# Kernel optimization log

Hardware: AMD Instinct MI355X
Metric: run time of the kernel (lower is better)

Reference implementation:

```python
import jax, jax.numpy as jnp
import numpy as np


def setup_inputs() -> dict:
    key = jax.random.key(0)
    k1, k2, k3, k4 = jax.random.split(key, 4)
    B, C, H, W = 16, 64, 128, 128
    x = jax.random.normal(k1, (B, C, H, W), dtype=jnp.float32)
    y = jax.random.normal(k2, (B, C, H, W), dtype=jnp.float32)
    # nn.Parameter(torch.zeros(1)) in the original; use small random values so
    # the attention branch contributes (zeros would make it a pure residual).
    temperature1 = jax.random.normal(k3, (1,), dtype=jnp.float32) * 0.1
    temperature2 = jax.random.normal(k4, (1,), dtype=jnp.float32) * 0.1
    return {"x": x, "y": y, "temperature1": temperature1,
            "temperature2": temperature2, "num_heads": 4}


def _l2norm_lastdim(v):
    # F.normalize(v, dim=-1): v / max(||v||_2, eps)
    n = jnp.sqrt(jnp.sum(v * v, axis=-1, keepdims=True))
    return v / jnp.maximum(n, 1e-12)


def reference(x, y, temperature1, temperature2, num_heads):
    B, C, H, W = x.shape
    c = C // num_heads
    HW = H * W
    # b (head c) h w -> b head c (h w)
    xr = x.reshape(B, num_heads, c, HW)
    yr = y.reshape(B, num_heads, c, HW)

    # key_x normalized over (h w); key_y (b head (hw) c) normalized over dim=-2,
    # which is the same (h w) axis of yr in 'bhck' layout.
    key_x = _l2norm_lastdim(xr)
    key_y = _l2norm_lastdim(yr)
    # energy[b,h,c,d] = sum_k key_x[b,h,c,k] * key_y[b,h,d,k]  -> (B, head, c, c)
    energy = jnp.einsum('bhck,bhdk->bhcd', key_x, key_y)

    attn1 = jax.nn.softmax(energy, axis=-1)                        # (B,h,c,c)
    attn2 = jax.nn.softmax(energy.transpose(0, 1, 3, 2), axis=-1)  # (B,h,c,c)

    # y_att (b head (hw) c) = value_y @ attn1, then 'b head (h w) c -> b (head c) h w'
    # out[b,h,d,k] = sum_c attn1[b,h,c,d] * yr[b,h,c,k]
    y_att = jnp.einsum('bhcd,bhck->bhdk', attn1, yr).reshape(B, C, H, W)
    x_att = jnp.einsum('bhcd,bhck->bhdk', attn2, xr).reshape(B, C, H, W)

    y_ = temperature1[0] * y_att + x
    x_ = temperature2[0] * x_att + y
    return jnp.concatenate((x_, y_), axis=1)  # (B, 2C, H, W)
```

## Files before the change

### kernel.cpp

```cpp
#include <hip/hip_runtime.h>

#define HW    16384
#define CPH   16
#define NBH   64
#define KSLICE 2048
#define TKT   256
#define LS    260
#define KPT   4

#define WS_SX   16384
#define WS_SY   17408
#define WS_W    18432
#define WS_ZERO_BYTES (18432 * 4)

__global__ __launch_bounds__(256) void gram_kernel(
    const float* __restrict__ x,
    const float* __restrict__ y,
    float* __restrict__ ws)
{
    __shared__ float xs[16 * LS];
    __shared__ float ys[16 * LS];
    __shared__ float Gs[256];
    __shared__ float sxs[16], sys[16];

    const int blk = blockIdx.x;
    const int bh  = blk >> 3;
    const int ks  = (blk & 7) * KSLICE;
    const int t   = threadIdx.x;

    Gs[t] = 0.f;
    if (t < 16) { sxs[t] = 0.f; sys[t] = 0.f; }

    const int c0 = t & 3;
    const int d0 = (t >> 2) & 3;
    const int g  = t >> 4;

    float acc[4][4];
    #pragma unroll
    for (int i = 0; i < 4; ++i)
        #pragma unroll
        for (int j = 0; j < 4; ++j) acc[i][j] = 0.f;
    float sqx[4] = {0.f, 0.f, 0.f, 0.f};
    float sqy[4] = {0.f, 0.f, 0.f, 0.f};

    const float* xb = x + (size_t)bh * CPH * HW + ks;
    const float* yb = y + (size_t)bh * CPH * HW + ks;

    for (int kt = 0; kt < KSLICE; kt += TKT) {
        __syncthreads();
        #pragma unroll
        for (int i = 0; i < 4; ++i) {
            int idx = i * 256 + t;
            int row = idx >> 6;
            int col = (idx & 63) * 4;
            float4 xv = *reinterpret_cast<const float4*>(xb + (size_t)row * HW + kt + col);
            float4 yv = *reinterpret_cast<const float4*>(yb + (size_t)row * HW + kt + col);
            *reinterpret_cast<float4*>(&xs[row * LS + col]) = xv;
            *reinterpret_cast<float4*>(&ys[row * LS + col]) = yv;
        }
        __syncthreads();

        #pragma unroll
        for (int kq = 0; kq < 16; kq += 4) {
            float4 xr[4], yr[4];
            #pragma unroll
            for (int i = 0; i < 4; ++i)
                xr[i] = *reinterpret_cast<const float4*>(&xs[(c0 + 4 * i) * LS + g * 16 + kq]);
            #pragma unroll
            for (int j = 0; j < 4; ++j)
                yr[j] = *reinterpret_cast<const float4*>(&ys[(d0 + 4 * j) * LS + g * 16 + kq]);
            #pragma unroll
            for (int i = 0; i < 4; ++i)
                #pragma unroll
                for (int j = 0; j < 4; ++j) {
                    acc[i][j] = fmaf(xr[i].x, yr[j].x, acc[i][j]);
                    acc[i][j] = fmaf(xr[i].y, yr[j].y, acc[i][j]);
                    acc[i][j] = fmaf(xr[i].z, yr[j].z, acc[i][j]);
                    acc[i][j] = fmaf(xr[i].w, yr[j].w, acc[i][j]);
                }
            if (d0 == 0) {
                #pragma unroll
                for (int i = 0; i < 4; ++i) {
                    sqx[i] = fmaf(xr[i].x, xr[i].x, sqx[i]);
                    sqx[i] = fmaf(xr[i].y, xr[i].y, sqx[i]);
                    sqx[i] = fmaf(xr[i].z, xr[i].z, sqx[i]);
                    sqx[i] = fmaf(xr[i].w, xr[i].w, sqx[i]);
                }
            }
            if (c0 == 0) {
                #pragma unroll
                for (int j = 0; j < 4; ++j) {
                    sqy[j] = fmaf(yr[j].x, yr[j].x, sqy[j]);
                    sqy[j] = fmaf(yr[j].y, yr[j].y, sqy[j]);
                    sqy[j] = fmaf(yr[j].z, yr[j].z, sqy[j]);
                    sqy[j] = fmaf(yr[j].w, yr[j].w, sqy[j]);
                }
            }
        }
    }

    #pragma unroll
    for (int i = 0; i < 4; ++i)
        #pragma unroll
        for (int j = 0; j < 4; ++j)
            atomicAdd(&Gs[(c0 + 4 * i) * 16 + (d0 + 4 * j)], acc[i][j]);
    if (d0 == 0) {
        #pragma unroll
        for (int i = 0; i < 4; ++i) atomicAdd(&sxs[c0 + 4 * i], sqx[i]);
    }
    if (c0 == 0) {
        #pragma unroll
        for (int j = 0; j < 4; ++j) atomicAdd(&sys[d0 + 4 * j], sqy[j]);
    }
    __syncthreads();
    atomicAdd(&ws[bh * 256 + t], Gs[t]);
    if (t < 16)       atomicAdd(&ws[WS_SX + bh * 16 + t], sxs[t]);
    else if (t < 32)  atomicAdd(&ws[WS_SY + bh * 16 + (t - 16)], sys[t - 16]);
}

__global__ __launch_bounds__(256) void softmax_kernel(
    float* __restrict__ ws,
    const float* __restrict__ t1p,
    const float* __restrict__ t2p)
{
    const int bh = blockIdx.x;
    const int t  = threadIdx.x;
    const int i  = t >> 4;
    const int j  = t & 15;

    __shared__ float Es[256];

    float nx = fmaxf(sqrtf(ws[WS_SX + bh * 16 + i]), 1e-12f);
    float ny = fmaxf(sqrtf(ws[WS_SY + bh * 16 + j]), 1e-12f);
    float e  = ws[bh * 256 + i * 16 + j] / (nx * ny);
    Es[t] = e;
    __syncthreads();

    float rm = -1e30f;
    #pragma unroll
    for (int r = 0; r < 16; ++r) rm = fmaxf(rm, Es[i * 16 + r]);
    float rs = 0.f;
    #pragma unroll
    for (int r = 0; r < 16; ++r) rs += expf(Es[i * 16 + r] - rm);
    float a1 = expf(e - rm) / rs;

    float cm = -1e30f;
    #pragma unroll
    for (int r = 0; r < 16; ++r) cm = fmaxf(cm, Es[r * 16 + j]);
    float cs = 0.f;
    #pragma unroll
    for (int r = 0; r < 16; ++r) cs += expf(Es[r * 16 + j] - cm);
    float v2 = expf(e - cm) / cs;

    const float t1 = t1p[0];
    const float t2 = t2p[0];

    float* W = ws + WS_W + bh * 512;
    W[(i * 16 + j) * 2 + 1] = t1 * a1;
    W[(j * 16 + i) * 2 + 0] = t2 * v2;
}

__global__ __launch_bounds__(256) void apply_kernel(
    const float* __restrict__ x,
    const float* __restrict__ y,
    const float* __restrict__ ws,
    float* __restrict__ out)
{
    const int CHUNKS = HW / (256 * KPT);
    const int blk   = blockIdx.x;
    const int bh    = blk / CHUNKS;
    const int chunk = blk % CHUNKS;
    const int t     = threadIdx.x;
    const int k0    = chunk * (256 * KPT) + t * KPT;

    __shared__ float2 Ws[256];
    Ws[t] = reinterpret_cast<const float2*>(ws + WS_W)[bh * 256 + t];
    __syncthreads();

    const int b = bh >> 2;
    const int h = bh & 3;

    const float* xbase = x + ((size_t)bh * CPH) * HW + k0;
    const float* ybase = y + ((size_t)bh * CPH) * HW + k0;

    float accx[16][KPT];
    float accy[16][KPT];
    #pragma unroll
    for (int d = 0; d < 16; ++d)
        #pragma unroll
        for (int j = 0; j < KPT; ++j) { accx[d][j] = 0.f; accy[d][j] = 0.f; }

    float4 xq = *reinterpret_cast<const float4*>(xbase);
    float4 yq = *reinterpret_cast<const float4*>(ybase);
    #pragma unroll
    for (int c = 0; c < 16; ++c) {
        float4 xn, yn;
        if (c < 15) {
            xn = *reinterpret_cast<const float4*>(xbase + (size_t)(c + 1) * HW);
            yn = *reinterpret_cast<const float4*>(ybase + (size_t)(c + 1) * HW);
        }
        float xv[KPT] = {xq.x, xq.y, xq.z, xq.w};
        float yv[KPT] = {yq.x, yq.y, yq.z, yq.w};
        #pragma unroll
        for (int d = 0; d < 16; ++d) {
            float2 w = Ws[c * 16 + d];
            #pragma unroll
            for (int j = 0; j < KPT; ++j) accx[d][j] = fmaf(w.x, xv[j], accx[d][j]);
            #pragma unroll
            for (int j = 0; j < KPT; ++j) accy[d][j] = fmaf(w.y, yv[j], accy[d][j]);
        }
        #pragma unroll
        for (int j = 0; j < KPT; ++j) accx[c][j] += yv[j];
        #pragma unroll
        for (int j = 0; j < KPT; ++j) accy[c][j] += xv[j];
        xq = xn; yq = yn;
    }

    const size_t obx = ((size_t)b * 128 + h * 16) * HW + k0;
    const size_t oby = obx + (size_t)64 * HW;
    #pragma unroll
    for (int d = 0; d < 16; ++d) {
        float4 px = make_float4(accx[d][0], accx[d][1], accx[d][2], accx[d][3]);
        float4 py = make_float4(accy[d][0], accy[d][1], accy[d][2], accy[d][3]);
        *reinterpret_cast<float4*>(out + obx + (size_t)d * HW) = px;
        *reinterpret_cast<float4*>(out + oby + (size_t)d * HW) = py;
    }
}

extern "C" void kernel_launch(void* const* d_in, const int* in_sizes, int n_in,
                              void* d_out, int out_size, void* d_ws, size_t ws_size,
                              hipStream_t stream) {
    const float* x  = (const float*)d_in[0];
    const float* y  = (const float*)d_in[1];
    const float* t1 = (const float*)d_in[2];
    const float* t2 = (const float*)d_in[3];
    float* ws  = (float*)d_ws;
    float* out = (float*)d_out;

    hipMemsetAsync(d_ws, 0, WS_ZERO_BYTES, stream);
    gram_kernel<<<NBH * 8, 256, 0, stream>>>(x, y, ws);
    softmax_kernel<<<NBH, 256, 0, stream>>>(ws, t1, t2);
    apply_kernel<<<NBH * (HW / (256 * KPT)), 256, 0, stream>>>(x, y, ws, out);
}
```

Baseline: 278.6 us.

## Fuse softmax into apply kernel, replace atomics with partial sums, drop memset

```diff
diff --git a/kernel.cpp b/kernel.cpp
--- a/kernel.cpp
+++ b/kernel.cpp
@@ -1,17 +1,17 @@
 #include <hip/hip_runtime.h>
 
-#define HW    16384
-#define CPH   16
-#define NBH   64
-#define KSLICE 2048
-#define TKT   256
-#define LS    260
-#define KPT   4
-
-#define WS_SX   16384
-#define WS_SY   17408
-#define WS_W    18432
-#define WS_ZERO_BYTES (18432 * 4)
+#define HW     16384
+#define CPH    16
+#define NBH    64
+#define NS     16
+#define KSLICE (HW/NS)
+#define TKT    256
+#define LS     260
+#define KPT    4
+
+#define WS_GP   0
+#define WS_SXP  262144
+#define WS_SYP  278528
 
 __global__ __launch_bounds__(256) void gram_kernel(
     const float* __restrict__ x,
@@ -24,8 +24,9 @@
     __shared__ float sxs[16], sys[16];
 
     const int blk = blockIdx.x;
-    const int bh  = blk >> 3;
-    const int ks  = (blk & 7) * KSLICE;
+    const int bh  = blk >> 4;
+    const int sl  = blk & (NS - 1);
+    const int ks  = sl * KSLICE;
     const int t   = threadIdx.x;
 
     Gs[t] = 0.f;
@@ -113,57 +114,17 @@
         for (int j = 0; j < 4; ++j) atomicAdd(&sys[d0 + 4 * j], sqy[j]);
     }
     __syncthreads();
-    atomicAdd(&ws[bh * 256 + t], Gs[t]);
-    if (t < 16)       atomicAdd(&ws[WS_SX + bh * 16 + t], sxs[t]);
-    else if (t < 32)  atomicAdd(&ws[WS_SY + bh * 16 + (t - 16)], sys[t - 16]);
-}
-
-__global__ __launch_bounds__(256) void softmax_kernel(
-    float* __restrict__ ws,
-    const float* __restrict__ t1p,
-    const float* __restrict__ t2p)
-{
-    const int bh = blockIdx.x;
-    const int t  = threadIdx.x;
-    const int i  = t >> 4;
-    const int j  = t & 15;
-
-    __shared__ float Es[256];
-
-    float nx = fmaxf(sqrtf(ws[WS_SX + bh * 16 + i]), 1e-12f);
-    float ny = fmaxf(sqrtf(ws[WS_SY + bh * 16 + j]), 1e-12f);
-    float e  = ws[bh * 256 + i * 16 + j] / (nx * ny);
-    Es[t] = e;
-    __syncthreads();
-
-    float rm = -1e30f;
-    #pragma unroll
-    for (int r = 0; r < 16; ++r) rm = fmaxf(rm, Es[i * 16 + r]);
-    float rs = 0.f;
-    #pragma unroll
-    for (int r = 0; r < 16; ++r) rs += expf(Es[i * 16 + r] - rm);
-    float a1 = expf(e - rm) / rs;
-
-    float cm = -1e30f;
-    #pragma unroll
-    for (int r = 0; r < 16; ++r) cm = fmaxf(cm, Es[r * 16 + j]);
-    float cs = 0.f;
-    #pragma unroll
-    for (int r = 0; r < 16; ++r) cs += expf(Es[r * 16 + j] - cm);
-    float v2 = expf(e - cm) / cs;
-
-    const float t1 = t1p[0];
-    const float t2 = t2p[0];
-
-    float* W = ws + WS_W + bh * 512;
-    W[(i * 16 + j) * 2 + 1] = t1 * a1;
-    W[(j * 16 + i) * 2 + 0] = t2 * v2;
+    ws[WS_GP + (bh * NS + sl) * 256 + t] = Gs[t];
+    if (t < 16)       ws[WS_SXP + (bh * NS + sl) * 16 + t]        = sxs[t];
+    else if (t < 32)  ws[WS_SYP + (bh * NS + sl) * 16 + (t - 16)] = sys[t - 16];
 }
 
 __global__ __launch_bounds__(256) void apply_kernel(
     const float* __restrict__ x,
     const float* __restrict__ y,
     const float* __restrict__ ws,
+    const float* __restrict__ t1p,
+    const float* __restrict__ t2p,
     float* __restrict__ out)
 {
     const int CHUNKS = HW / (256 * KPT);
@@ -171,14 +132,66 @@
     const int bh    = blk / CHUNKS;
     const int chunk = blk % CHUNKS;
     const int t     = threadIdx.x;
-    const int k0    = chunk * (256 * KPT) + t * KPT;
-
-    __shared__ float2 Ws[256];
-    Ws[t] = reinterpret_cast<const float2*>(ws + WS_W)[bh * 256 + t];
-    __syncthreads();
-
-    const int b = bh >> 2;
-    const int h = bh & 3;
+    const int i     = t >> 4;
+    const int j     = t & 15;
+
+    __shared__ float Es[256];
+    __shared__ float SXs[16], SYs[16];
+    __shared__ float W1s[256], W2s[256];
+
+    {
+        float gsum = 0.f;
+        const float* gp = ws + WS_GP + bh * NS * 256 + t;
+        #pragma unroll
+        for (int s = 0; s < NS; ++s) gsum += gp[s * 256];
+        if (t < 16) {
+            float v = 0.f;
+            const float* p = ws + WS_SXP + bh * NS * 16 + t;
+            #pragma unroll
+            for (int s = 0; s < NS; ++s) v += p[s * 16];
+            SXs[t] = v;
+        } else if (t < 32) {
+            float v = 0.f;
+            const float* p = ws + WS_SYP + bh * NS * 16 + (t - 16);
+            #pragma unroll
+            for (int s = 0; s < NS; ++s) v += p[s * 16];
+            SYs[t - 16] = v;
+        }
+        Es[t] = gsum;
+        __syncthreads();
+
+        float nx = fmaxf(sqrtf(SXs[i]), 1e-12f);
+        float ny = fmaxf(sqrtf(SYs[j]), 1e-12f);
+        float e  = Es[t] / (nx * ny);
+        Es[t] = e;
+        __syncthreads();
+
+        float rm = -1e30f;
+        #pragma unroll
+        for (int r = 0; r < 16; ++r) rm = fmaxf(rm, Es[i * 16 + r]);
+        float rs = 0.f;
+        #pragma unroll
+        for (int r = 0; r < 16; ++r) rs += expf(Es[i * 16 + r] - rm);
+        float a1 = expf(e - rm) / rs;
+
+        float cm = -1e30f;
+        #pragma unroll
+        for (int r = 0; r < 16; ++r) cm = fmaxf(cm, Es[r * 16 + j]);
+        float cs = 0.f;
+        #pragma unroll
+        for (int r = 0; r < 16; ++r) cs += expf(Es[r * 16 + j] - cm);
+        float v2 = expf(e - cm) / cs;
+
+        const float t1 = t1p[0];
+        const float t2 = t2p[0];
+        W1s[i * 16 + j] = t1 * a1;
+        W2s[j * 16 + i] = t2 * v2;
+        __syncthreads();
+    }
+
+    const int k0 = chunk * (256 * KPT) + t * KPT;
+    const int b  = bh >> 2;
+    const int h  = bh & 3;
 
     const float* xbase = x + ((size_t)bh * CPH) * HW + k0;
     const float* ybase = y + ((size_t)bh * CPH) * HW + k0;
@@ -188,7 +201,7 @@
     #pragma unroll
     for (int d = 0; d < 16; ++d)
         #pragma unroll
-        for (int j = 0; j < KPT; ++j) { accx[d][j] = 0.f; accy[d][j] = 0.f; }
+        for (int q = 0; q < KPT; ++q) { accx[d][q] = 0.f; accy[d][q] = 0.f; }
 
     float4 xq = *reinterpret_cast<const float4*>(xbase);
     float4 yq = *reinterpret_cast<const float4*>(ybase);
@@ -203,16 +216,17 @@
         float yv[KPT] = {yq.x, yq.y, yq.z, yq.w};
         #pragma unroll
         for (int d = 0; d < 16; ++d) {
-            float2 w = Ws[c * 16 + d];
-            #pragma unroll
-            for (int j = 0; j < KPT; ++j) accx[d][j] = fmaf(w.x, xv[j], accx[d][j]);
-            #pragma unroll
-            for (int j = 0; j < KPT; ++j) accy[d][j] = fmaf(w.y, yv[j], accy[d][j]);
-        }
-        #pragma unroll
-        for (int j = 0; j < KPT; ++j) accx[c][j] += yv[j];
-        #pragma unroll
-        for (int j = 0; j < KPT; ++j) accy[c][j] += xv[j];
+            float w2 = W2s[c * 16 + d];
+            float w1 = W1s[c * 16 + d];
+            #pragma unroll
+            for (int q = 0; q < KPT; ++q) accx[d][q] = fmaf(w2, xv[q], accx[d][q]);
+            #pragma unroll
+            for (int q = 0; q < KPT; ++q) accy[d][q] = fmaf(w1, yv[q], accy[d][q]);
+        }
+        #pragma unroll
+        for (int q = 0; q < KPT; ++q) accx[c][q] += yv[q];
+        #pragma unroll
+        for (int q = 0; q < KPT; ++q) accy[c][q] += xv[q];
         xq = xn; yq = yn;
     }
 
@@ -237,8 +251,6 @@
     float* ws  = (float*)d_ws;
     float* out = (float*)d_out;
 
-    hipMemsetAsync(d_ws, 0, WS_ZERO_BYTES, stream);
-    gram_kernel<<<NBH * 8, 256, 0, stream>>>(x, y, ws);
-    softmax_kernel<<<NBH, 256, 0, stream>>>(ws, t1, t2);
-    apply_kernel<<<NBH * (HW / (256 * KPT)), 256, 0, stream>>>(x, y, ws, out);
+    gram_kernel<<<NBH * NS, 256, 0, stream>>>(x, y, ws);
+    apply_kernel<<<NBH * (HW / (256 * KPT)), 256, 0, stream>>>(x, y, ws, t1, t2, out);
 }
```

Measured after the change: 293.4 us. 1.05x slower.
